# Performance work log

Measured on AMD Instinct MI355X. Metric: run time of the kernel, lower is better.

The kernel has to match this reference:

```python
import jax, jax.numpy as jnp
import numpy as np


def setup_inputs() -> dict:
    key = jax.random.key(0)
    k1, k2 = jax.random.split(key)
    N, D = 8192, 256
    cond_feature = jax.random.normal(k1, (N, D), dtype=jnp.float32)
    sol_feature = jax.random.normal(k2, (N, D), dtype=jnp.float32)
    temperature = jnp.asarray(0.5, dtype=jnp.float32)  # learned scalar, used as exp(temperature)
    return {"cond_feature": cond_feature, "sol_feature": sol_feature, "temperature": temperature}


def reference(cond_feature, sol_feature, temperature):
    N = cond_feature.shape[0]
    c = cond_feature.reshape(N, -1)  # [N, D]
    s = sol_feature.reshape(sol_feature.shape[0], -1)  # [N, D]
    # pairwise L2 distance via ||a||^2 + ||b||^2 - 2 a.b (avoids N x N x D intermediate)
    c2 = jnp.sum(c * c, axis=-1)  # [N]
    s2 = jnp.sum(s * s, axis=-1)  # [N]
    d2 = c2[:, None] + s2[None, :] - 2.0 * jnp.einsum('nd,md->nm', c, s)
    dist = jnp.sqrt(jnp.maximum(d2, 0.0))  # [N, N]
    sim = -dist * jnp.exp(temperature)
    # cross_entropy(sim, arange) + cross_entropy(sim.T, arange): diagonal of log-softmax both ways
    logp_row = jax.nn.log_softmax(sim, axis=-1)  # CE over rows
    logp_col = jax.nn.log_softmax(sim, axis=0)   # CE over columns == CE(sim.T, labels)
    diag = jnp.arange(N)
    loss_row = -jnp.mean(logp_row[diag, diag])
    loss_col = -jnp.mean(logp_col[diag, diag])
    return (loss_row + loss_col) * 0.5
```

## Files before the change

kernel.cpp:

```cpp
#include <hip/hip_runtime.h>
#include <math.h>

#define DIM 256
#define TM 256
#define TN 128
#define BK 64

typedef float f32x4 __attribute__((ext_vector_type(4)));
typedef long long2v __attribute__((ext_vector_type(2)));

typedef const __attribute__((address_space(1))) void* gas_ptr;
typedef __attribute__((address_space(3))) void* las_ptr;

__device__ __forceinline__ void async_cp16(const void* g, void* l) {
    __builtin_amdgcn_global_load_lds((gas_ptr)g, (las_ptr)l, 16, 0, 0);
}

__global__ __launch_bounds__(256) void convert_kernel(
        const float* __restrict__ C, const float* __restrict__ S,
        unsigned char* __restrict__ Cb, unsigned char* __restrict__ Sb,
        float* __restrict__ c2, float* __restrict__ s2,
        float* __restrict__ ddot, float* __restrict__ sums0,
        float* __restrict__ out, int N) {
    int gtid = blockIdx.x * 256 + threadIdx.x;
    if (gtid < 2 * N) sums0[gtid] = 0.0f;
    if (gtid == 0) out[0] = 0.0f;
    int row = gtid >> 6;
    int l = gtid & 63;
    if (row >= N) return;
    float4 v  = ((const float4*)(C + (size_t)row * DIM))[l];
    float4 sv = ((const float4*)(S + (size_t)row * DIM))[l];
    int pc = __builtin_amdgcn_cvt_pk_fp8_f32(v.x, v.y, 0, false);
    pc     = __builtin_amdgcn_cvt_pk_fp8_f32(v.z, v.w, pc, true);
    int ps = __builtin_amdgcn_cvt_pk_fp8_f32(sv.x, sv.y, 0, false);
    ps     = __builtin_amdgcn_cvt_pk_fp8_f32(sv.z, sv.w, ps, true);
    int idx4 = (l >> 4) * 16 + ((l & 7) >> 1) * 4 + ((l & 15) >> 3) * 2 + (l & 1);
    ((int*)(Cb + (size_t)row * DIM))[idx4] = pc;
    ((int*)(Sb + (size_t)row * DIM))[idx4] = ps;
    float nc = v.x * v.x + v.y * v.y + v.z * v.z + v.w * v.w;
    float ns = sv.x * sv.x + sv.y * sv.y + sv.z * sv.z + sv.w * sv.w;
    float cr = v.x * sv.x + v.y * sv.y + v.z * sv.z + v.w * sv.w;
    #pragma unroll
    for (int off = 32; off > 0; off >>= 1) {
        nc += __shfl_down(nc, off, 64);
        ns += __shfl_down(ns, off, 64);
        cr += __shfl_down(cr, off, 64);
    }
    if (l == 0) { c2[row] = nc; s2[row] = ns; ddot[row] = cr; }
}

__global__ __launch_bounds__(512, 4) void mfma_kernel(
        const unsigned char* __restrict__ Cb, const unsigned char* __restrict__ Sb,
        const float* __restrict__ c2, const float* __restrict__ s2,
        const float* __restrict__ temp,
        float* __restrict__ rowsum, float* __restrict__ colsum, int N) {
    __shared__ __align__(16) unsigned char Abuf[TM * BK];
    __shared__ __align__(16) unsigned char Bbuf[TN * BK];
    __shared__ float rs[TM], cs[TN], c2t[TM], s2t[TN];

    const int tid = threadIdx.x;
    const int bm = blockIdx.y * TM;
    const int bn = blockIdx.x * TN;
    const int w  = tid >> 6;
    const int l  = tid & 63;
    const int wm = (w >> 1) * 64;
    const int wn = (w & 1) * 64;

    const float escale = __expf(temp[0]);
    const float Kf = escale * 1.4426950408889634f;
    const float K2 = Kf * Kf;
    const float m2K2 = -2.0f * K2;

    if (tid < TM) { rs[tid] = 0.0f; c2t[tid] = K2 * c2[bm + tid]; }
    else if (tid < TM + TN) {
        int t = tid - TM; cs[t] = 0.0f; s2t[t] = K2 * s2[bn + t];
    }

    const int l4 = l >> 2;
    const int sc = (l & 3) ^ (l4 & 3);
    const unsigned char* gA = Cb + (size_t)(bm + w * 16 + l4) * DIM + sc * 16;
    const unsigned char* gB = Sb + (size_t)(bn + w * 16 + l4) * DIM + sc * 16;
    unsigned char* lA = &Abuf[w * 1024];
    unsigned char* lB = &Bbuf[w * 1024];
    const size_t askip = (size_t)128 * DIM;

    const int m16 = l & 15;
    const int q = l >> 4;
    int aoff[4], boff[4];
    #pragma unroll
    for (int i = 0; i < 4; ++i) {
        aoff[i] = (wm + i * 16 + m16) * BK + ((q ^ (m16 & 3)) * 16);
        boff[i] = (wn + i * 16 + m16) * BK + ((q ^ (m16 & 3)) * 16);
    }

    f32x4 acc[4][4] = {};

    #pragma unroll
    for (int kk = 0; kk < 4; ++kk) {
        async_cp16(gA, lA);
        async_cp16(gA + askip, lA + 8192);
        async_cp16(gB, lB);
        gA += BK; gB += BK;
        __syncthreads();

        long2v af[4], bf[4];
        #pragma unroll
        for (int i = 0; i < 4; ++i) af[i] = *(const long2v*)&Abuf[aoff[i]];
        #pragma unroll
        for (int j = 0; j < 4; ++j) bf[j] = *(const long2v*)&Bbuf[boff[j]];
        #pragma unroll
        for (int mi = 0; mi < 4; ++mi)
            #pragma unroll
            for (int ni = 0; ni < 4; ++ni) {
                acc[mi][ni] = __builtin_amdgcn_mfma_f32_16x16x32_fp8_fp8(
                    af[mi].x, bf[ni].x, acc[mi][ni], 0, 0, 0);
                acc[mi][ni] = __builtin_amdgcn_mfma_f32_16x16x32_fp8_fp8(
                    af[mi].y, bf[ni].y, acc[mi][ni], 0, 0, 0);
            }
        __syncthreads();
    }

    float c2v[4][4], s2v[4];
    #pragma unroll
    for (int mi = 0; mi < 4; ++mi)
        #pragma unroll
        for (int r = 0; r < 4; ++r) c2v[mi][r] = c2t[wm + mi * 16 + q * 4 + r];
    #pragma unroll
    for (int ni = 0; ni < 4; ++ni) s2v[ni] = s2t[wn + ni * 16 + m16];

    float rp[16];
    #pragma unroll
    for (int s = 0; s < 16; ++s) rp[s] = 0.0f;
    float cp[4] = {0.f, 0.f, 0.f, 0.f};

    #pragma unroll
    for (int mi = 0; mi < 4; ++mi) {
        #pragma unroll
        for (int ni = 0; ni < 4; ++ni) {
            #pragma unroll
            for (int r = 0; r < 4; ++r) {
                float d2 = fmaf(m2K2, acc[mi][ni][r], c2v[mi][r] + s2v[ni]);
                d2 = fmaxf(d2, 0.0f);
                float e = __builtin_amdgcn_exp2f(-__builtin_amdgcn_sqrtf(d2));
                rp[mi * 4 + r] += e;
                cp[ni] += e;
            }
        }
    }

    #pragma unroll
    for (int b = 0; b < 4; ++b) {
        const int n = 16 >> b;
        const int bit = (m16 >> b) & 1;
        #pragma unroll
        for (int k = 0; k < 8; ++k) {
            if (k < (n >> 1)) {
                float keep = bit ? rp[2 * k + 1] : rp[2 * k];
                float send = bit ? rp[2 * k] : rp[2 * k + 1];
                float recv = __shfl_xor(send, 1 << b, 64);
                rp[k] = keep + recv;
            }
        }
    }
    const int myrow = wm + (m16 >> 2) * 16 + q * 4 + (m16 & 3);
    atomicAdd(&rs[myrow], rp[0]);

    #pragma unroll
    for (int b = 0; b < 2; ++b) {
        const int n = 4 >> b;
        const int bit = (q >> b) & 1;
        #pragma unroll
        for (int k = 0; k < 2; ++k) {
            if (k < (n >> 1)) {
                float keep = bit ? cp[2 * k + 1] : cp[2 * k];
                float send = bit ? cp[2 * k] : cp[2 * k + 1];
                float recv = __shfl_xor(send, 16 << b, 64);
                cp[k] = keep + recv;
            }
        }
    }
    const int mycol = wn + q * 16 + m16;
    atomicAdd(&cs[mycol], cp[0]);

    __syncthreads();
    if (tid < TM) atomicAdd(&rowsum[bm + tid], rs[tid]);
    else if (tid < TM + TN) atomicAdd(&colsum[bn + tid - TM], cs[tid - TM]);
}

__global__ __launch_bounds__(256) void finalize_kernel(
        const float* __restrict__ rowsum, const float* __restrict__ colsum,
        const float* __restrict__ c2, const float* __restrict__ s2,
        const float* __restrict__ ddot, const float* __restrict__ temp,
        float* __restrict__ out, int N) {
    __shared__ float red[4];
    const float escale = __expf(temp[0]);
    const int tid = threadIdx.x;
    int i = blockIdx.x * 256 + tid;
    float sum = 0.0f;
    if (i < N) {
        float d2 = c2[i] + s2[i] - 2.0f * ddot[i];
        float dist = __builtin_amdgcn_sqrtf(fmaxf(d2, 0.0f));
        sum = __logf(rowsum[i]) + __logf(colsum[i]) + 2.0f * escale * dist;
    }
    #pragma unroll
    for (int off = 32; off > 0; off >>= 1) sum += __shfl_down(sum, off, 64);
    if ((tid & 63) == 0) red[tid >> 6] = sum;
    __syncthreads();
    if (tid == 0)
        atomicAdd(out, (red[0] + red[1] + red[2] + red[3]) / (2.0f * (float)N));
}

extern "C" void kernel_launch(void* const* d_in, const int* in_sizes, int n_in,
                              void* d_out, int out_size, void* d_ws, size_t ws_size,
                              hipStream_t stream) {
    const float* C = (const float*)d_in[0];
    const float* S = (const float*)d_in[1];
    const float* T = (const float*)d_in[2];
    const int N = in_sizes[0] / DIM;

    float* ws     = (float*)d_ws;
    float* c2     = ws;
    float* s2     = ws + N;
    float* rowsum = ws + 2 * N;
    float* colsum = ws + 3 * N;
    float* ddot   = ws + 4 * N;
    unsigned char* Cb = (unsigned char*)(ws + 5 * N + 64);
    unsigned char* Sb = Cb + (size_t)N * DIM;

    convert_kernel<<<(N * 64) / 256, 256, 0, stream>>>(
        C, S, Cb, Sb, c2, s2, ddot, rowsum, (float*)d_out, N);

    dim3 grid(N / TN, N / TM);
    mfma_kernel<<<grid, 512, 0, stream>>>(
        Cb, Sb, c2, s2, T, rowsum, colsum, N);

    finalize_kernel<<<(N + 255) / 256, 256, 0, stream>>>(
        rowsum, colsum, c2, s2, ddot, T, (float*)d_out, N);
}
```

Baseline: 112.5 us.

## Switch to 32x32x64 scaled FP8 MFMA with pre-tiled operand layout

Replaces the 16x16x32 FP8 MFMA pairs with the gfx950 scaled 32x32x64 f8f6f4 MFMA (unit scales). The convert kernel now writes FP8 operands in a 32-row blocked layout that matches the MFMA fragment order. Tiles can then be copied to LDS contiguously and read as 32-byte fragments without swizzling. The goal is fewer MFMA issues and less LDS address math. The epilogue is rewritten for the 16-element accumulator layout, and correctness depends on the new layout mapping being exact.

```diff
diff --git a/kernel.cpp b/kernel.cpp
--- a/kernel.cpp
+++ b/kernel.cpp
@@ -4,10 +4,10 @@
 #define DIM 256
 #define TM 256
 #define TN 128
-#define BK 64
-
-typedef float f32x4 __attribute__((ext_vector_type(4)));
-typedef long long2v __attribute__((ext_vector_type(2)));
+
+typedef int   v4i   __attribute__((ext_vector_type(4)));
+typedef int   v8i   __attribute__((ext_vector_type(8)));
+typedef float f32x16 __attribute__((ext_vector_type(16)));
 
 typedef const __attribute__((address_space(1))) void* gas_ptr;
 typedef __attribute__((address_space(3))) void* las_ptr;
@@ -34,9 +34,10 @@
     pc     = __builtin_amdgcn_cvt_pk_fp8_f32(v.z, v.w, pc, true);
     int ps = __builtin_amdgcn_cvt_pk_fp8_f32(sv.x, sv.y, 0, false);
     ps     = __builtin_amdgcn_cvt_pk_fp8_f32(sv.z, sv.w, ps, true);
-    int idx4 = (l >> 4) * 16 + ((l & 7) >> 1) * 4 + ((l & 15) >> 3) * 2 + (l & 1);
-    ((int*)(Cb + (size_t)row * DIM))[idx4] = pc;
-    ((int*)(Sb + (size_t)row * DIM))[idx4] = ps;
+    int idx4 = (row >> 5) * 2048 + (l >> 4) * 512 + ((l >> 2) & 1) * 256
+             + ((row & 31) + 32 * ((l >> 3) & 1)) * 4 + (l & 3);
+    ((int*)Cb)[idx4] = pc;
+    ((int*)Sb)[idx4] = ps;
     float nc = v.x * v.x + v.y * v.y + v.z * v.z + v.w * v.w;
     float ns = sv.x * sv.x + sv.y * sv.y + sv.z * sv.z + sv.w * sv.w;
     float cr = v.x * sv.x + v.y * sv.y + v.z * sv.z + v.w * sv.w;
@@ -54,8 +55,8 @@
         const float* __restrict__ c2, const float* __restrict__ s2,
         const float* __restrict__ temp,
         float* __restrict__ rowsum, float* __restrict__ colsum, int N) {
-    __shared__ __align__(16) unsigned char Abuf[TM * BK];
-    __shared__ __align__(16) unsigned char Bbuf[TN * BK];
+    __shared__ __align__(16) unsigned char Abuf[TM * 64];
+    __shared__ __align__(16) unsigned char Bbuf[TN * 64];
     __shared__ float rs[TM], cs[TN], c2t[TM], s2t[TN];
 
     const int tid = threadIdx.x;
@@ -76,111 +77,102 @@
         int t = tid - TM; cs[t] = 0.0f; s2t[t] = K2 * s2[bn + t];
     }
 
-    const int l4 = l >> 2;
-    const int sc = (l & 3) ^ (l4 & 3);
-    const unsigned char* gA = Cb + (size_t)(bm + w * 16 + l4) * DIM + sc * 16;
-    const unsigned char* gB = Sb + (size_t)(bn + w * 16 + l4) * DIM + sc * 16;
-    unsigned char* lA = &Abuf[w * 1024];
-    unsigned char* lB = &Bbuf[w * 1024];
-    const size_t askip = (size_t)128 * DIM;
-
-    const int m16 = l & 15;
-    const int q = l >> 4;
-    int aoff[4], boff[4];
-    #pragma unroll
-    for (int i = 0; i < 4; ++i) {
-        aoff[i] = (wm + i * 16 + m16) * BK + ((q ^ (m16 & 3)) * 16);
-        boff[i] = (wn + i * 16 + m16) * BK + ((q ^ (m16 & 3)) * 16);
-    }
-
-    f32x4 acc[4][4] = {};
+    const unsigned char* gA = Cb + (size_t)((bm >> 5) + w) * 8192 + (size_t)l * 16;
+    const unsigned char* gB = Sb + (size_t)((bn >> 5) + (w >> 1)) * 8192
+                                 + (size_t)(w & 1) * 1024 + (size_t)l * 16;
+    unsigned char* lA = &Abuf[w * 2048];
+    unsigned char* lB = &Bbuf[(w >> 1) * 2048 + (w & 1) * 1024];
+
+    const int abase = (w >> 1) * 4096 + l * 16;
+    const int bbase = (w & 1) * 4096 + l * 16;
+
+    f32x16 acc[2][2] = {};
 
     #pragma unroll
     for (int kk = 0; kk < 4; ++kk) {
         async_cp16(gA, lA);
-        async_cp16(gA + askip, lA + 8192);
+        async_cp16(gA + 1024, lA + 1024);
         async_cp16(gB, lB);
-        gA += BK; gB += BK;
+        gA += 2048; gB += 2048;
         __syncthreads();
 
-        long2v af[4], bf[4];
-        #pragma unroll
-        for (int i = 0; i < 4; ++i) af[i] = *(const long2v*)&Abuf[aoff[i]];
-        #pragma unroll
-        for (int j = 0; j < 4; ++j) bf[j] = *(const long2v*)&Bbuf[boff[j]];
-        #pragma unroll
-        for (int mi = 0; mi < 4; ++mi)
+        v8i af[2], bf[2];
+        #pragma unroll
+        for (int t = 0; t < 2; ++t) {
+            v4i alo = *(const v4i*)&Abuf[abase + t * 2048];
+            v4i ahi = *(const v4i*)&Abuf[abase + t * 2048 + 1024];
+            af[t] = __builtin_shufflevector(alo, ahi, 0, 1, 2, 3, 4, 5, 6, 7);
+            v4i blo = *(const v4i*)&Bbuf[bbase + t * 2048];
+            v4i bhi = *(const v4i*)&Bbuf[bbase + t * 2048 + 1024];
+            bf[t] = __builtin_shufflevector(blo, bhi, 0, 1, 2, 3, 4, 5, 6, 7);
+        }
+        #pragma unroll
+        for (int mi = 0; mi < 2; ++mi)
             #pragma unroll
-            for (int ni = 0; ni < 4; ++ni) {
-                acc[mi][ni] = __builtin_amdgcn_mfma_f32_16x16x32_fp8_fp8(
-                    af[mi].x, bf[ni].x, acc[mi][ni], 0, 0, 0);
-                acc[mi][ni] = __builtin_amdgcn_mfma_f32_16x16x32_fp8_fp8(
-                    af[mi].y, bf[ni].y, acc[mi][ni], 0, 0, 0);
-            }
+            for (int ni = 0; ni < 2; ++ni)
+                acc[mi][ni] = __builtin_amdgcn_mfma_scale_f32_32x32x64_f8f6f4(
+                    af[mi], bf[ni], acc[mi][ni], 0, 0,
+                    0, 0x7F, 0, 0x7F);
         __syncthreads();
     }
 
-    float c2v[4][4], s2v[4];
-    #pragma unroll
-    for (int mi = 0; mi < 4; ++mi)
-        #pragma unroll
-        for (int r = 0; r < 4; ++r) c2v[mi][r] = c2t[wm + mi * 16 + q * 4 + r];
-    #pragma unroll
-    for (int ni = 0; ni < 4; ++ni) s2v[ni] = s2t[wn + ni * 16 + m16];
-
-    float rp[16];
-    #pragma unroll
-    for (int s = 0; s < 16; ++s) rp[s] = 0.0f;
-    float cp[4] = {0.f, 0.f, 0.f, 0.f};
-
-    #pragma unroll
-    for (int mi = 0; mi < 4; ++mi) {
-        #pragma unroll
-        for (int ni = 0; ni < 4; ++ni) {
+    const int q2 = l >> 5;
+    const int col5 = l & 31;
+    float s2v[2] = { s2t[wn + col5], s2t[wn + 32 + col5] };
+
+    float rfold[2];
+    float cp[2] = {0.f, 0.f};
+
+    #pragma unroll
+    for (int mi = 0; mi < 2; ++mi) {
+        float c2r[16];
+        #pragma unroll
+        for (int s = 0; s < 16; ++s)
+            c2r[s] = c2t[wm + mi * 32 + (s & 3) + 8 * (s >> 2) + 4 * q2];
+        float rp[16];
+        #pragma unroll
+        for (int s = 0; s < 16; ++s) rp[s] = 0.0f;
+        #pragma unroll
+        for (int ni = 0; ni < 2; ++ni) {
             #pragma unroll
-            for (int r = 0; r < 4; ++r) {
-                float d2 = fmaf(m2K2, acc[mi][ni][r], c2v[mi][r] + s2v[ni]);
+            for (int s = 0; s < 16; ++s) {
+                float d2 = fmaf(m2K2, acc[mi][ni][s], c2r[s] + s2v[ni]);
                 d2 = fmaxf(d2, 0.0f);
                 float e = __builtin_amdgcn_exp2f(-__builtin_amdgcn_sqrtf(d2));
-                rp[mi * 4 + r] += e;
+                rp[s] += e;
                 cp[ni] += e;
             }
         }
-    }
-
-    #pragma unroll
-    for (int b = 0; b < 4; ++b) {
-        const int n = 16 >> b;
-        const int bit = (m16 >> b) & 1;
-        #pragma unroll
-        for (int k = 0; k < 8; ++k) {
-            if (k < (n >> 1)) {
-                float keep = bit ? rp[2 * k + 1] : rp[2 * k];
-                float send = bit ? rp[2 * k] : rp[2 * k + 1];
-                float recv = __shfl_xor(send, 1 << b, 64);
-                rp[k] = keep + recv;
+        #pragma unroll
+        for (int b = 0; b < 4; ++b) {
+            const int n = 16 >> b;
+            const int bit = (l >> b) & 1;
+            #pragma unroll
+            for (int k = 0; k < 8; ++k) {
+                if (k < (n >> 1)) {
+                    float keep = bit ? rp[2 * k + 1] : rp[2 * k];
+                    float send = bit ? rp[2 * k] : rp[2 * k + 1];
+                    rp[k] = keep + __shfl_xor(send, 1 << b, 64);
+                }
             }
         }
-    }
-    const int myrow = wm + (m16 >> 2) * 16 + q * 4 + (m16 & 3);
-    atomicAdd(&rs[myrow], rp[0]);
-
-    #pragma unroll
-    for (int b = 0; b < 2; ++b) {
-        const int n = 4 >> b;
-        const int bit = (q >> b) & 1;
-        #pragma unroll
-        for (int k = 0; k < 2; ++k) {
-            if (k < (n >> 1)) {
-                float keep = bit ? cp[2 * k + 1] : cp[2 * k];
-                float send = bit ? cp[2 * k] : cp[2 * k + 1];
-                float recv = __shfl_xor(send, 16 << b, 64);
-                cp[k] = keep + recv;
-            }
-        }
-    }
-    const int mycol = wn + q * 16 + m16;
-    atomicAdd(&cs[mycol], cp[0]);
+        rfold[mi] = rp[0];
+    }
+    const int mymi = (l >> 4) & 1;
+    {
+        float keep = mymi ? rfold[1] : rfold[0];
+        float send = mymi ? rfold[0] : rfold[1];
+        float rfin = keep + __shfl_xor(send, 16, 64);
+        const int s = l & 15;
+        const int myrow = wm + mymi * 32 + (s & 3) + 8 * (s >> 2) + 4 * q2;
+        atomicAdd(&rs[myrow], rfin);
+    }
+    {
+        float keep = q2 ? cp[1] : cp[0];
+        float send = q2 ? cp[0] : cp[1];
+        float cfin = keep + __shfl_xor(send, 32, 64);
+        atomicAdd(&cs[wn + q2 * 32 + col5], cfin);
+    }
 
     __syncthreads();
     if (tid < TM) atomicAdd(&rowsum[bm + tid], rs[tid]);
```

New measurement: 113.4 us. About the same (+0.8%).
